# Optimization experiments

Hardware: AMD Instinct MI355X
Metric: run time of the kernel (lower is better)

The kernel has to match this reference:

```python
import jax, jax.numpy as jnp
import numpy as np
import math

DIM_IN = 2
DIM_HIDDEN = 64
DIM_OUT = 16
NUM_LAYERS = 5  # num_layers-1 = 4 hidden SirenLayers per subnet + 1 last layer
W0 = 30.0
W0_INITIAL = 30.0
S0 = 0.0
C = 6.0
N_POINTS = 262144


def wire(w0, s0, z):
    # sin(w0*z) * exp(-(s0*z)^2)
    return jnp.sin(w0 * z) * jnp.exp(-jnp.square(s0 * z))


def setup_inputs() -> dict:
    key = jax.random.key(0)
    ks = jax.random.split(key, 8)
    # NOTE: source passes is_first=False for every layer, so init bound is
    # sqrt(c/dim_in)/layer_w0 for ALL layers (including the first).
    std0 = math.sqrt(C / DIM_IN) / W0_INITIAL
    stdh = math.sqrt(C / DIM_HIDDEN) / W0
    stdl = math.sqrt(C / DIM_HIDDEN) / W0
    u = lambda k, shape, s: jax.random.uniform(k, shape, jnp.float32, -s, s)
    nmid = NUM_LAYERS - 2  # hidden->hidden layers per subnet (3)
    return {
        "x": jax.random.uniform(ks[0], (N_POINTS, DIM_IN), jnp.float32),
        "W0m": u(ks[1], (DIM_OUT, DIM_HIDDEN, DIM_IN), std0),
        "b0": u(ks[2], (DIM_OUT, DIM_HIDDEN), std0),
        "Wm": u(ks[3], (nmid, DIM_OUT, DIM_HIDDEN, DIM_HIDDEN), stdh),
        "bm": u(ks[4], (nmid, DIM_OUT, DIM_HIDDEN), stdh),
        "Wl": u(ks[5], (DIM_OUT, DIM_HIDDEN), stdl),
        "bl": u(ks[6], (DIM_OUT,), stdl),
    }


def reference(x, W0m, b0, Wm, bm, Wl, bl):
    # First layer of each subnet (uses w0_initial): [N,D] x [O,H,D] -> [N,O,H]
    h = wire(W0_INITIAL, S0, jnp.einsum("nd,ohd->noh", x, W0m) + b0)
    # Middle hidden layers (w0), scanned over the fixed layer stack.
    def body(h, wb):
        W, b = wb
        h = wire(W0, S0, jnp.einsum("noh,ogh->nog", h, W) + b)
        return h, None
    h, _ = jax.lax.scan(body, h, (Wm, bm))
    # Last layer per subnet: dim 1 output each, is_last -> +0.5, no activation.
    out = jnp.einsum("noh,oh->no", h, Wl) + bl + 0.5  # [N, dim_out]
    return out
```

## Files before the change

kernel.cpp:

```cpp
#include <hip/hip_runtime.h>

typedef short bf16x8 __attribute__((ext_vector_type(8)));
typedef float f32x16 __attribute__((ext_vector_type(16)));

#define NBGROUPS 96
#define NTILES   8192
#define SCALE 4.7746482927568601f

union Frag  { bf16x8 v; unsigned u[4]; uint4 q; };
union AccLd { float4 f4[4]; f32x16 v; };

__device__ __forceinline__ unsigned pk_bf16(float lo, float hi) {
    unsigned r;
    asm("v_cvt_pk_bf16_f32 %0, %1, %2" : "=v"(r) : "v"(lo), "v"(hi));
    return r;
}
__device__ __forceinline__ float lo_f(unsigned w) { return __uint_as_float(w << 16); }
__device__ __forceinline__ float hi_f(unsigned w) { return __uint_as_float(w & 0xffff0000u); }

__device__ __forceinline__ float sin_rev(float z) {
    float v  = z - rintf(z);
    float v2 = v * v;
    float p  = 32.765379f;
    p = fmaf(p, v2, -74.468884f);
    p = fmaf(p, v2,  81.365064f);
    p = fmaf(p, v2, -41.331084f);
    p = fmaf(p, v2,   6.2830526f);
    return p * v;
}

__device__ __forceinline__ void init_acc(f32x16* acc, const float4* ldsBias, int Lb, int hi) {
#pragma unroll
    for (int tg = 0; tg < 2; ++tg) {
        AccLd a;
        const float4* base = &ldsBias[((Lb*2+tg)*2 + hi)*4];
#pragma unroll
        for (int q = 0; q < 4; ++q) a.f4[q] = base[q];
        acc[tg] = a.v;
    }
}

__device__ __forceinline__ void transitionHL(const f32x16* acc, Frag* Bhi, Frag* Blo) {
#pragma unroll
    for (int tg = 0; tg < 2; ++tg) {
        float sv[16];
#pragma unroll
        for (int r = 0; r < 16; ++r) sv[r] = sin_rev(acc[tg][r]);
#pragma unroll
        for (int s = 0; s < 2; ++s)
#pragma unroll
            for (int wi = 0; wi < 4; ++wi) {
                float a = sv[s*8 + 2*wi], b = sv[s*8 + 2*wi + 1];
                unsigned ph = pk_bf16(a, b);
                Bhi[tg*2+s].u[wi] = ph;
                Blo[tg*2+s].u[wi] = pk_bf16(a - lo_f(ph), b - hi_f(ph));
            }
    }
}

__global__ __launch_bounds__(256, 2)
void siren_kernel(const float* __restrict__ x, const float* __restrict__ W0m,
                  const float* __restrict__ b0, const float* __restrict__ Wm,
                  const float* __restrict__ bm, const float* __restrict__ Wl,
                  const float* __restrict__ bl, float* __restrict__ out)
{
    __shared__ uint4  ldsAhi[3*2*4*64];
    __shared__ uint4  ldsAlo[3*2*4*64];
    __shared__ float4 ldsBias[4*2*2*4];
    __shared__ float  ldsWl[2][32];

    const int tid  = threadIdx.x;
    const int pg   = blockIdx.x;
    const int o    = blockIdx.y;
    const int lane = tid & 63;
    const int wv   = tid >> 6;
    const int col  = lane & 31;
    const int hi   = lane >> 5;

    for (int idx = tid; idx < 3*2*4*64; idx += 256) {
        int l2  = idx & 63;
        int fi  = idx >> 6;
        int c   = fi & 3;
        int tg  = (fi >> 2) & 1;
        int L   = fi >> 3;
        int hi2 = l2 >> 5;
        int g   = tg*32 + (l2 & 31);
        int th  = c >> 1, s = c & 1;
        const float2* Wrow2 = (const float2*)(Wm + (((size_t)(L*16 + o)*64 + g)*64));
        uint4 whi, wlo;
        unsigned* uh = (unsigned*)&whi;
        unsigned* ul = (unsigned*)&wlo;
#pragma unroll
        for (int wi = 0; wi < 4; ++wi) {
            int h = th*32 + s*16 + 8*(wi>>1) + 2*(wi&1) + 4*hi2;
            float2 wp = Wrow2[h >> 1];
            float a = SCALE*wp.x, b = SCALE*wp.y;
            unsigned ph = pk_bf16(a, b);
            uh[wi] = ph;
            ul[wi] = pk_bf16(a - lo_f(ph), b - hi_f(ph));
        }
        ldsAhi[idx] = whi;
        ldsAlo[idx] = wlo;
    }
    if (tid < 64) {
        int q   = tid & 3;
        int hi2 = (tid >> 2) & 1;
        int tg  = (tid >> 3) & 1;
        int Lb  = tid >> 4;
        int h0  = tg*32 + 8*q + 4*hi2;
        const float* bsrc = (Lb < 3) ? (bm + (Lb*16 + o)*64) : (b0 + o*64);
        ldsBias[tid] = make_float4(SCALE*bsrc[h0], SCALE*bsrc[h0+1],
                                   SCALE*bsrc[h0+2], SCALE*bsrc[h0+3]);
    }
    if (tid >= 64 && tid < 128) {
        int t2  = tid - 64;
        int hi2 = t2 >> 5;
        int idx = t2 & 31;
        int tg  = idx >> 4;
        int r   = idx & 15;
        int s = r >> 3, j = r & 7;
        int h = tg*32 + 16*s + (j & 3) + 8*(j >> 2) + 4*hi2;
        ldsWl[hi2][idx] = Wl[o*64 + h];
    }

    Frag L1A[2];
#pragma unroll
    for (int tg = 0; tg < 2; ++tg) {
        int g = tg*32 + col;
        float2 wp = ((const float2*)W0m)[o*64 + g];
        float s0 = SCALE*wp.x, s1 = SCALE*wp.y;
        unsigned u0 = pk_bf16(s0, s0), u1 = pk_bf16(s1, s1);
        float l0 = s0 - lo_f(u0), l1 = s1 - lo_f(u1);
        L1A[tg].u[0] = hi ? 0u : u0;
        L1A[tg].u[1] = hi ? 0u : u1;
        L1A[tg].u[2] = hi ? 0u : pk_bf16(l0, l0);
        L1A[tg].u[3] = hi ? 0u : pk_bf16(l1, l1);
    }
    const float blv = bl[o] + 0.5f;

    __syncthreads();

    const int tend = ((pg + 1) * NTILES) / NBGROUPS;
    for (int t = (pg * NTILES) / NBGROUPS + wv; t < tend; t += 4) {
        const int pp = t*32 + col;

        float2 xv = ((const float2*)x)[pp];
        unsigned ux = pk_bf16(xv.x, xv.y);
        float x0h = lo_f(ux), x1h = hi_f(ux);
        unsigned w0 = pk_bf16(x0h, xv.x - x0h);
        unsigned w1 = pk_bf16(x1h, xv.y - x1h);
        Frag B1;
        B1.u[0] = hi ? 0u : w0;
        B1.u[1] = hi ? 0u : w1;
        B1.u[2] = hi ? 0u : w0;
        B1.u[3] = hi ? 0u : w1;

        f32x16 acc[2];
        init_acc(acc, ldsBias, 3, hi);
        acc[0] = __builtin_amdgcn_mfma_f32_32x32x16_bf16(L1A[0].v, B1.v, acc[0], 0, 0, 0);
        acc[1] = __builtin_amdgcn_mfma_f32_32x32x16_bf16(L1A[1].v, B1.v, acc[1], 0, 0, 0);

        Frag Bhi[4], Blo[4];
        transitionHL(acc, Bhi, Blo);

#pragma unroll
        for (int L = 0; L < 3; ++L) {
            init_acc(acc, ldsBias, L, hi);
#pragma unroll
            for (int c = 0; c < 4; ++c) {
                Frag Ah0, Ah1, Al0, Al1;
                Ah0.q = ldsAhi[((L*2+0)*4+c)*64 + lane];
                Ah1.q = ldsAhi[((L*2+1)*4+c)*64 + lane];
                Al0.q = ldsAlo[((L*2+0)*4+c)*64 + lane];
                Al1.q = ldsAlo[((L*2+1)*4+c)*64 + lane];
                acc[0] = __builtin_amdgcn_mfma_f32_32x32x16_bf16(Ah0.v, Bhi[c].v, acc[0], 0, 0, 0);
                acc[1] = __builtin_amdgcn_mfma_f32_32x32x16_bf16(Ah1.v, Bhi[c].v, acc[1], 0, 0, 0);
                acc[0] = __builtin_amdgcn_mfma_f32_32x32x16_bf16(Ah0.v, Blo[c].v, acc[0], 0, 0, 0);
                acc[1] = __builtin_amdgcn_mfma_f32_32x32x16_bf16(Ah1.v, Blo[c].v, acc[1], 0, 0, 0);
                acc[0] = __builtin_amdgcn_mfma_f32_32x32x16_bf16(Al0.v, Bhi[c].v, acc[0], 0, 0, 0);
                acc[1] = __builtin_amdgcn_mfma_f32_32x32x16_bf16(Al1.v, Bhi[c].v, acc[1], 0, 0, 0);
            }
            if (L < 2) transitionHL(acc, Bhi, Blo);
        }

        const float4* wl4 = (const float4*)&ldsWl[hi][0];
        float sum = 0.f;
#pragma unroll
        for (int tg = 0; tg < 2; ++tg)
#pragma unroll
            for (int q = 0; q < 4; ++q) {
                float4 w4 = wl4[tg*4 + q];
                sum = fmaf(sin_rev(acc[tg][q*4+0]), w4.x, sum);
                sum = fmaf(sin_rev(acc[tg][q*4+1]), w4.y, sum);
                sum = fmaf(sin_rev(acc[tg][q*4+2]), w4.z, sum);
                sum = fmaf(sin_rev(acc[tg][q*4+3]), w4.w, sum);
            }
        sum += __shfl_xor(sum, 32);
        if (lane < 32) out[(size_t)pp*16 + o] = sum + blv;
    }
}

extern "C" void kernel_launch(void* const* d_in, const int* in_sizes, int n_in,
                              void* d_out, int out_size, void* d_ws, size_t ws_size,
                              hipStream_t stream) {
    (void)in_sizes; (void)n_in; (void)out_size; (void)d_ws; (void)ws_size;
    siren_kernel<<<dim3(NBGROUPS, 16), dim3(256), 0, stream>>>(
        (const float*)d_in[0], (const float*)d_in[1], (const float*)d_in[2],
        (const float*)d_in[3], (const float*)d_in[4], (const float*)d_in[5],
        (const float*)d_in[6], (float*)d_out);
}
```

Baseline: 394.6 us.

## Interleave two tiles per wave, packed sin, drop last-layer lo split

Each wave now processes two 32-point tiles at once so their MFMA chains interleave and hide latency. The sine polynomial is written on float2 vectors so it can map to packed FP32 instructions. The last hidden layer drops the hi/lo bf16 split for both the activations and the weights, which cuts that layer's MFMAs from six to two per chunk and shrinks LDS. The grid becomes 128 groups with a fixed 8-iteration loop. The price is lower accuracy in the last hidden layer and higher register pressure from the doubled accumulators.

```diff
diff --git a/kernel.cpp b/kernel.cpp
--- a/kernel.cpp
+++ b/kernel.cpp
@@ -2,9 +2,9 @@
 
 typedef short bf16x8 __attribute__((ext_vector_type(8)));
 typedef float f32x16 __attribute__((ext_vector_type(16)));
-
-#define NBGROUPS 96
-#define NTILES   8192
+typedef float f32x2  __attribute__((ext_vector_type(2)));
+
+#define NBGROUPS 128
 #define SCALE 4.7746482927568601f
 
 union Frag  { bf16x8 v; unsigned u[4]; uint4 q; };
@@ -18,14 +18,15 @@
 __device__ __forceinline__ float lo_f(unsigned w) { return __uint_as_float(w << 16); }
 __device__ __forceinline__ float hi_f(unsigned w) { return __uint_as_float(w & 0xffff0000u); }
 
-__device__ __forceinline__ float sin_rev(float z) {
-    float v  = z - rintf(z);
-    float v2 = v * v;
-    float p  = 32.765379f;
-    p = fmaf(p, v2, -74.468884f);
-    p = fmaf(p, v2,  81.365064f);
-    p = fmaf(p, v2, -41.331084f);
-    p = fmaf(p, v2,   6.2830526f);
+__device__ __forceinline__ f32x2 sin2(f32x2 z) {
+    f32x2 r  = { rintf(z.x), rintf(z.y) };
+    f32x2 v  = z - r;
+    f32x2 v2 = v * v;
+    f32x2 p  = { 32.765379f, 32.765379f };
+    p = __builtin_elementwise_fma(p, v2, (f32x2){-74.468884f, -74.468884f});
+    p = __builtin_elementwise_fma(p, v2, (f32x2){ 81.365064f,  81.365064f});
+    p = __builtin_elementwise_fma(p, v2, (f32x2){-41.331084f, -41.331084f});
+    p = __builtin_elementwise_fma(p, v2, (f32x2){  6.2830526f,  6.2830526f});
     return p * v;
 }
 
@@ -42,20 +43,27 @@
 
 __device__ __forceinline__ void transitionHL(const f32x16* acc, Frag* Bhi, Frag* Blo) {
 #pragma unroll
-    for (int tg = 0; tg < 2; ++tg) {
-        float sv[16];
-#pragma unroll
-        for (int r = 0; r < 16; ++r) sv[r] = sin_rev(acc[tg][r]);
-#pragma unroll
-        for (int s = 0; s < 2; ++s)
-#pragma unroll
-            for (int wi = 0; wi < 4; ++wi) {
-                float a = sv[s*8 + 2*wi], b = sv[s*8 + 2*wi + 1];
-                unsigned ph = pk_bf16(a, b);
-                Bhi[tg*2+s].u[wi] = ph;
-                Blo[tg*2+s].u[wi] = pk_bf16(a - lo_f(ph), b - hi_f(ph));
-            }
-    }
+    for (int tg = 0; tg < 2; ++tg)
+#pragma unroll
+        for (int j = 0; j < 8; ++j) {
+            f32x2 z = { acc[tg][2*j], acc[tg][2*j+1] };
+            f32x2 s = sin2(z);
+            unsigned ph = pk_bf16(s.x, s.y);
+            f32x2 hf = { lo_f(ph), hi_f(ph) };
+            f32x2 d  = s - hf;
+            Bhi[tg*2 + (j>>2)].u[j&3] = ph;
+            Blo[tg*2 + (j>>2)].u[j&3] = pk_bf16(d.x, d.y);
+        }
+}
+__device__ __forceinline__ void transitionH(const f32x16* acc, Frag* Bhi) {
+#pragma unroll
+    for (int tg = 0; tg < 2; ++tg)
+#pragma unroll
+        for (int j = 0; j < 8; ++j) {
+            f32x2 z = { acc[tg][2*j], acc[tg][2*j+1] };
+            f32x2 s = sin2(z);
+            Bhi[tg*2 + (j>>2)].u[j&3] = pk_bf16(s.x, s.y);
+        }
 }
 
 __global__ __launch_bounds__(256, 2)
@@ -65,7 +73,7 @@
                   const float* __restrict__ bl, float* __restrict__ out)
 {
     __shared__ uint4  ldsAhi[3*2*4*64];
-    __shared__ uint4  ldsAlo[3*2*4*64];
+    __shared__ uint4  ldsAlo[2*2*4*64];
     __shared__ float4 ldsBias[4*2*2*4];
     __shared__ float  ldsWl[2][32];
 
@@ -100,7 +108,7 @@
             ul[wi] = pk_bf16(a - lo_f(ph), b - hi_f(ph));
         }
         ldsAhi[idx] = whi;
-        ldsAlo[idx] = wlo;
+        if (idx < 2*2*4*64) ldsAlo[idx] = wlo;
     }
     if (tid < 64) {
         int q   = tid & 3;
@@ -140,32 +148,47 @@
 
     __syncthreads();
 
-    const int tend = ((pg + 1) * NTILES) / NBGROUPS;
-    for (int t = (pg * NTILES) / NBGROUPS + wv; t < tend; t += 4) {
-        const int pp = t*32 + col;
-
-        float2 xv = ((const float2*)x)[pp];
-        unsigned ux = pk_bf16(xv.x, xv.y);
-        float x0h = lo_f(ux), x1h = hi_f(ux);
-        unsigned w0 = pk_bf16(x0h, xv.x - x0h);
-        unsigned w1 = pk_bf16(x1h, xv.y - x1h);
-        Frag B1;
-        B1.u[0] = hi ? 0u : w0;
-        B1.u[1] = hi ? 0u : w1;
-        B1.u[2] = hi ? 0u : w0;
-        B1.u[3] = hi ? 0u : w1;
-
-        f32x16 acc[2];
-        init_acc(acc, ldsBias, 3, hi);
-        acc[0] = __builtin_amdgcn_mfma_f32_32x32x16_bf16(L1A[0].v, B1.v, acc[0], 0, 0, 0);
-        acc[1] = __builtin_amdgcn_mfma_f32_32x32x16_bf16(L1A[1].v, B1.v, acc[1], 0, 0, 0);
-
-        Frag Bhi[4], Blo[4];
-        transitionHL(acc, Bhi, Blo);
-
-#pragma unroll
-        for (int L = 0; L < 3; ++L) {
-            init_acc(acc, ldsBias, L, hi);
+    const int tbase = pg*64 + wv;
+#pragma unroll 1
+    for (int k = 0; k < 8; ++k) {
+        const int ta  = tbase + 8*k;
+        const int ppa = ta*32 + col;
+        const int ppb = ppa + 128;
+
+        float2 xa = ((const float2*)x)[ppa];
+        float2 xb = ((const float2*)x)[ppb];
+        Frag B1a, B1b;
+        {
+            unsigned ux = pk_bf16(xa.x, xa.y);
+            float x0h = lo_f(ux), x1h = hi_f(ux);
+            unsigned w0 = pk_bf16(x0h, xa.x - x0h);
+            unsigned w1 = pk_bf16(x1h, xa.y - x1h);
+            B1a.u[0] = hi ? 0u : w0;  B1a.u[1] = hi ? 0u : w1;
+            B1a.u[2] = hi ? 0u : w0;  B1a.u[3] = hi ? 0u : w1;
+            ux = pk_bf16(xb.x, xb.y);
+            x0h = lo_f(ux); x1h = hi_f(ux);
+            w0 = pk_bf16(x0h, xb.x - x0h);
+            w1 = pk_bf16(x1h, xb.y - x1h);
+            B1b.u[0] = hi ? 0u : w0;  B1b.u[1] = hi ? 0u : w1;
+            B1b.u[2] = hi ? 0u : w0;  B1b.u[3] = hi ? 0u : w1;
+        }
+
+        f32x16 accA[2], accB[2];
+        init_acc(accA, ldsBias, 3, hi);
+        init_acc(accB, ldsBias, 3, hi);
+        accA[0] = __builtin_amdgcn_mfma_f32_32x32x16_bf16(L1A[0].v, B1a.v, accA[0], 0, 0, 0);
+        accA[1] = __builtin_amdgcn_mfma_f32_32x32x16_bf16(L1A[1].v, B1a.v, accA[1], 0, 0, 0);
+        accB[0] = __builtin_amdgcn_mfma_f32_32x32x16_bf16(L1A[0].v, B1b.v, accB[0], 0, 0, 0);
+        accB[1] = __builtin_amdgcn_mfma_f32_32x32x16_bf16(L1A[1].v, B1b.v, accB[1], 0, 0, 0);
+
+        Frag BhiA[4], BloA[4], BhiB[4], BloB[4];
+        transitionHL(accA, BhiA, BloA);
+        transitionHL(accB, BhiB, BloB);
+
+#pragma unroll
+        for (int L = 0; L < 2; ++L) {
+            init_acc(accA, ldsBias, L, hi);
+            init_acc(accB, ldsBias, L, hi);
 #pragma unroll
             for (int c = 0; c < 4; ++c) {
                 Frag Ah0, Ah1, Al0, Al1;
@@ -173,30 +196,61 @@
                 Ah1.q = ldsAhi[((L*2+1)*4+c)*64 + lane];
                 Al0.q = ldsAlo[((L*2+0)*4+c)*64 + lane];
                 Al1.q = ldsAlo[((L*2+1)*4+c)*64 + lane];
-                acc[0] = __builtin_amdgcn_mfma_f32_32x32x16_bf16(Ah0.v, Bhi[c].v, acc[0], 0, 0, 0);
-                acc[1] = __builtin_amdgcn_mfma_f32_32x32x16_bf16(Ah1.v, Bhi[c].v, acc[1], 0, 0, 0);
-                acc[0] = __builtin_amdgcn_mfma_f32_32x32x16_bf16(Ah0.v, Blo[c].v, acc[0], 0, 0, 0);
-                acc[1] = __builtin_amdgcn_mfma_f32_32x32x16_bf16(Ah1.v, Blo[c].v, acc[1], 0, 0, 0);
-                acc[0] = __builtin_amdgcn_mfma_f32_32x32x16_bf16(Al0.v, Bhi[c].v, acc[0], 0, 0, 0);
-                acc[1] = __builtin_amdgcn_mfma_f32_32x32x16_bf16(Al1.v, Bhi[c].v, acc[1], 0, 0, 0);
+                accA[0] = __builtin_amdgcn_mfma_f32_32x32x16_bf16(Ah0.v, BhiA[c].v, accA[0], 0, 0, 0);
+                accA[1] = __builtin_amdgcn_mfma_f32_32x32x16_bf16(Ah1.v, BhiA[c].v, accA[1], 0, 0, 0);
+                accB[0] = __builtin_amdgcn_mfma_f32_32x32x16_bf16(Ah0.v, BhiB[c].v, accB[0], 0, 0, 0);
+                accB[1] = __builtin_amdgcn_mfma_f32_32x32x16_bf16(Ah1.v, BhiB[c].v, accB[1], 0, 0, 0);
+                accA[0] = __builtin_amdgcn_mfma_f32_32x32x16_bf16(Ah0.v, BloA[c].v, accA[0], 0, 0, 0);
+                accA[1] = __builtin_amdgcn_mfma_f32_32x32x16_bf16(Ah1.v, BloA[c].v, accA[1], 0, 0, 0);
+                accB[0] = __builtin_amdgcn_mfma_f32_32x32x16_bf16(Ah0.v, BloB[c].v, accB[0], 0, 0, 0);
+                accB[1] = __builtin_amdgcn_mfma_f32_32x32x16_bf16(Ah1.v, BloB[c].v, accB[1], 0, 0, 0);
+                accA[0] = __builtin_amdgcn_mfma_f32_32x32x16_bf16(Al0.v, BhiA[c].v, accA[0], 0, 0, 0);
+                accA[1] = __builtin_amdgcn_mfma_f32_32x32x16_bf16(Al1.v, BhiA[c].v, accA[1], 0, 0, 0);
+                accB[0] = __builtin_amdgcn_mfma_f32_32x32x16_bf16(Al0.v, BhiB[c].v, accB[0], 0, 0, 0);
+                accB[1] = __builtin_amdgcn_mfma_f32_32x32x16_bf16(Al1.v, BhiB[c].v, accB[1], 0, 0, 0);
             }
-            if (L < 2) transitionHL(acc, Bhi, Blo);
-        }
-
-        const float4* wl4 = (const float4*)&ldsWl[hi][0];
-        float sum = 0.f;
+            if (L == 0) {
+                transitionHL(accA, BhiA, BloA);
+                transitionHL(accB, BhiB, BloB);
+            } else {
+                transitionH(accA, BhiA);
+                transitionH(accB, BhiB);
+            }
+        }
+
+        init_acc(accA, ldsBias, 2, hi);
+        init_acc(accB, ldsBias, 2, hi);
+#pragma unroll
+        for (int c = 0; c < 4; ++c) {
+            Frag Ah0, Ah1;
+            Ah0.q = ldsAhi[((2*2+0)*4+c)*64 + lane];
+            Ah1.q = ldsAhi[((2*2+1)*4+c)*64 + lane];
+            accA[0] = __builtin_amdgcn_mfma_f32_32x32x16_bf16(Ah0.v, BhiA[c].v, accA[0], 0, 0, 0);
+            accA[1] = __builtin_amdgcn_mfma_f32_32x32x16_bf16(Ah1.v, BhiA[c].v, accA[1], 0, 0, 0);
+            accB[0] = __builtin_amdgcn_mfma_f32_32x32x16_bf16(Ah0.v, BhiB[c].v, accB[0], 0, 0, 0);
+            accB[1] = __builtin_amdgcn_mfma_f32_32x32x16_bf16(Ah1.v, BhiB[c].v, accB[1], 0, 0, 0);
+        }
+
+        const f32x2* wl2 = (const f32x2*)&ldsWl[hi][0];
+        f32x2 sa = {0.f, 0.f}, sb = {0.f, 0.f};
 #pragma unroll
         for (int tg = 0; tg < 2; ++tg)
 #pragma unroll
-            for (int q = 0; q < 4; ++q) {
-                float4 w4 = wl4[tg*4 + q];
-                sum = fmaf(sin_rev(acc[tg][q*4+0]), w4.x, sum);
-                sum = fmaf(sin_rev(acc[tg][q*4+1]), w4.y, sum);
-                sum = fmaf(sin_rev(acc[tg][q*4+2]), w4.z, sum);
-                sum = fmaf(sin_rev(acc[tg][q*4+3]), w4.w, sum);
+            for (int j = 0; j < 8; ++j) {
+                f32x2 w = wl2[tg*8 + j];
+                f32x2 za = { accA[tg][2*j], accA[tg][2*j+1] };
+                f32x2 zb = { accB[tg][2*j], accB[tg][2*j+1] };
+                sa = __builtin_elementwise_fma(sin2(za), w, sa);
+                sb = __builtin_elementwise_fma(sin2(zb), w, sb);
             }
-        sum += __shfl_xor(sum, 32);
-        if (lane < 32) out[(size_t)pp*16 + o] = sum + blv;
+        float suma = sa.x + sa.y;
+        float sumb = sb.x + sb.y;
+        suma += __shfl_xor(suma, 32);
+        sumb += __shfl_xor(sumb, 32);
+        if (lane < 32) {
+            out[(size_t)ppa*16 + o] = suma + blv;
+            out[(size_t)ppb*16 + o] = sumb + blv;
+        }
     }
 }
 
```

New measurement: 345.0 us. 12.6% less time.
